# Kernel tuning notes

Measured on AMD Instinct MI355X. Metric: run time of the kernel, lower is better.

Reference implementation:

```python
import jax, jax.numpy as jnp
import numpy as np

N, E, E_LG, H, KGE, NUM_GRAPHS, N_ITER = 100000, 500000, 1000000, 128, 128, 1024, 2
EPS = 1e-5

def _prelu(x, a):
    return jnp.where(x >= 0, x, a * x)

def _seg_mean(vals, idx, num):
    s = jax.ops.segment_sum(vals, idx, num_segments=num)
    c = jax.ops.segment_sum(jnp.ones((vals.shape[0],), vals.dtype), idx, num_segments=num)
    return s / jnp.maximum(c, 1.0)[:, None]

def setup_inputs() -> dict:
    key = jax.random.key(0)
    ks = jax.random.split(key, 16)
    sc = 1.0 / np.sqrt(H)
    inp = {
        "x": jax.random.normal(ks[0], (N, H), jnp.float32),
        "edge_attr": jax.random.normal(ks[1], (E, H), jnp.float32),
        "edge_index": jax.random.randint(ks[2], (2, E), 0, N),
        "batch": jnp.sort(jax.random.randint(ks[3], (N,), 0, NUM_GRAPHS)),
        "line_graph_edge_index": jax.random.randint(ks[4], (2, E_LG), 0, E),
        # edge_update_net: Linear + PReLU + BatchNorm1d (eval mode)
        "W1": jax.random.normal(ks[5], (H, H), jnp.float32) * sc,
        "b1": jnp.zeros((H,), jnp.float32),
        "a1": jnp.full((1,), 0.25, jnp.float32),
        "bn_gamma": jnp.ones((H,), jnp.float32),
        "bn_beta": jnp.zeros((H,), jnp.float32),
        "bn_mean": jnp.zeros((H,), jnp.float32),
        "bn_var": jnp.ones((H,), jnp.float32),
        # GRU (single layer, single step)
        "w_ih": jax.random.normal(ks[6], (3 * H, H), jnp.float32) * sc,
        "w_hh": jax.random.normal(ks[7], (3 * H, H), jnp.float32) * sc,
        "b_ih": jnp.zeros((3 * H,), jnp.float32),
        "b_hh": jnp.zeros((3 * H,), jnp.float32),
        # DynamicAttention net
        "Wa1": jax.random.normal(ks[8], (H // 2, H), jnp.float32) * sc,
        "ba1": jnp.zeros((H // 2,), jnp.float32),
        "a2": jnp.full((1,), 0.25, jnp.float32),
        "Wa2": jax.random.normal(ks[9], (1, H // 2), jnp.float32) * (1.0 / np.sqrt(H // 2)),
        "ba2": jnp.zeros((1,), jnp.float32),
        # readout
        "Wr": jax.random.normal(ks[10], (KGE, H), jnp.float32) * sc,
        "br": jnp.zeros((KGE,), jnp.float32),
    }
    return inp

def reference(x, edge_attr, W1, b1, a1, bn_gamma, bn_beta, bn_mean, bn_var,
              w_ih, w_hh, b_ih, b_hh, Wa1, ba1, a2, Wa2, ba2, Wr, br,
              edge_index, batch, line_graph_edge_index):
    src, dst = edge_index[0], edge_index[1]
    l_src, l_dst = line_graph_edge_index[0], line_graph_edge_index[1]
    h = x  # GRU hidden state [N, H]
    for _ in range(N_ITER):
        # edge-to-edge message passing (node_to_edge_proj is Identity here)
        fused = edge_attr + (x[src] + x[dst]) * 0.5  # [E, H]
        agg = _seg_mean(fused[l_src], l_dst, E)      # scatter-mean over line graph
        upd = _prelu(agg @ W1.T + b1, a1)
        upd = (upd - bn_mean) * jax.lax.rsqrt(bn_var + EPS) * bn_gamma + bn_beta
        fused = fused + upd
        node_updates = _seg_mean(fused, dst, N)      # [N, H]
        # single GRU step
        gi = node_updates @ w_ih.T + b_ih
        gh = h @ w_hh.T + b_hh
        gi_r, gi_z, gi_n = jnp.split(gi, 3, axis=-1)
        gh_r, gh_z, gh_n = jnp.split(gh, 3, axis=-1)
        r = jax.nn.sigmoid(gi_r + gh_r)
        z = jax.nn.sigmoid(gi_z + gh_z)
        n = jnp.tanh(gi_n + r * gh_n)
        h = (1.0 - z) * n + z * h
        x = h
    # dynamic attention: per-graph scalar gate
    graph_repr = _seg_mean(x, batch, NUM_GRAPHS)     # [G, H]
    attn = jax.nn.sigmoid(_prelu(graph_repr @ Wa1.T + ba1, a2) @ Wa2.T + ba2)  # [G, 1]
    attended = x * attn[batch]
    graph_emb = jax.ops.segment_sum(attended, batch, num_segments=NUM_GRAPHS)
    graph_emb = graph_emb @ Wr.T + br
    return (x, graph_emb)
```

## Files before the change

kernel.cpp:

```cpp
#include <hip/hip_runtime.h>
#include <stdint.h>

#define H 128
#define G_NUM 1024
#define BN_EPS 1e-5f
#define IDXCAP 512

typedef unsigned int uint;
typedef unsigned short ushort;
typedef unsigned char uchar;
typedef __attribute__((ext_vector_type(8))) __bf16 bf16x8;
typedef __attribute__((ext_vector_type(8))) ushort ushort8;
typedef __attribute__((ext_vector_type(4))) float f32x4;
typedef __attribute__((ext_vector_type(2))) float f32x2;

__device__ __forceinline__ float b2f(ushort u){ return __uint_as_float(((uint)u) << 16); }
__device__ __forceinline__ ushort f2b(float f){
    uint u = __float_as_uint(f);
    u += 0x7FFFu + ((u >> 16) & 1u);
    return (ushort)(u >> 16);
}
__device__ __forceinline__ float ldf(const void* p, size_t i, int bf){
    return bf ? b2f(((const ushort*)p)[i]) : ((const float*)p)[i];
}
__device__ __forceinline__ int swz(int r, int byte_in_row){
    return (r * 256 + byte_in_row) ^ ((r & 7) << 4);
}

#define GBODY(SRC, sA, sB) do{ \
    uint4 wA_ = *(const uint4*)((SRC) + (size_t)(sA) * H + ch16 * 8); \
    uint4 wB_ = *(const uint4*)((SRC) + (size_t)(sB) * H + ch16 * 8); \
    uint wa_[4] = {wA_.x, wA_.y, wA_.z, wA_.w}; \
    uint wb_[4] = {wB_.x, wB_.y, wB_.z, wB_.w}; \
    _Pragma("unroll") \
    for (int k2 = 0; k2 < 4; k2++){ \
        f32x2 va_, vb_; \
        va_.x = __uint_as_float(wa_[k2] << 16); va_.y = __uint_as_float(wa_[k2] & 0xFFFF0000u); \
        vb_.x = __uint_as_float(wb_[k2] << 16); vb_.y = __uint_as_float(wb_[k2] & 0xFFFF0000u); \
        accA[k2] += va_; accB[k2] += vb_; \
    } }while(0)

__global__ void k_setup_small(const uint* __restrict__ gamma_bits,
                              const void* b1, const void* a1, const void* gam, const void* bet,
                              const void* mean, const void* var, const void* bih, const void* bhh,
                              float* __restrict__ ep, float* __restrict__ bi, float* __restrict__ bh,
                              int* __restrict__ flag, ushort* __restrict__ fz1, ushort* __restrict__ fz2,
                              size_t zoff, int* __restrict__ lg_off, int E, int ELG,
                              int* __restrict__ nd_off, int N, int Etot){
    __shared__ int bfs;
    int t = threadIdx.x;
    if (t == 0){
        int f = (gamma_bits[0] == 0x3F803F80u) ? 1 : 0;
        *flag = f; bfs = f;
        lg_off[E] = ELG;
        nd_off[N] = Etot;
    }
    __syncthreads();
    int bf = bfs;
    bi[t] = ldf(bih, t, bf);
    bh[t] = ldf(bhh, t, bf);
    if (t < 128){
        ep[t]       = ldf(b1, t, bf);
        ep[128 + t] = rsqrtf(ldf(var, t, bf) + BN_EPS) * ldf(gam, t, bf);
        ep[256 + t] = ldf(mean, t, bf);
        ep[384 + t] = ldf(bet, t, bf);
        fz1[zoff + t] = 0; fz2[zoff + t] = 0;
    }
    if (t == 0) ep[512] = ldf(a1, 0, bf);
}

__global__ __launch_bounds__(256) void k_count_nd(const int* __restrict__ ei, int* __restrict__ cnt, int E){
    int t = blockIdx.x * 256 + threadIdx.x;
    if (t < E) atomicAdd(&cnt[ei[E + t]], 1);
}
__global__ __launch_bounds__(256) void k_fill_nd(const int* __restrict__ ei, const int* __restrict__ off,
                                                 int* __restrict__ cur, int* __restrict__ list, int E){
    int t = blockIdx.x * 256 + threadIdx.x;
    if (t >= E) return;
    int k = ei[E + t];
    int pos = atomicAdd(&cur[k], 1);
    list[off[k] + pos] = t;
}
__global__ __launch_bounds__(256) void k_rank(const int* __restrict__ nd_list, int* __restrict__ rank,
                                              int2* __restrict__ eis, const int* __restrict__ ei, int E){
    int j = blockIdx.x * 256 + threadIdx.x;
    if (j >= E) return;
    int e = nd_list[j];
    rank[e] = j;
    eis[j] = make_int2(ei[e], ei[E + e]);
}
__global__ __launch_bounds__(256) void k_count_lg(const int* __restrict__ lgi, const int* __restrict__ rank,
                                                  int* __restrict__ cnt, int ELG){
    int t = blockIdx.x * 256 + threadIdx.x;
    if (t < ELG) atomicAdd(&cnt[rank[lgi[ELG + t]]], 1);
}
__global__ __launch_bounds__(256) void k_fill_lg(const int* __restrict__ lgi, const int* __restrict__ rank,
                                                 const int* __restrict__ off, int* __restrict__ cur,
                                                 int* __restrict__ list, int ELG){
    int t = blockIdx.x * 256 + threadIdx.x;
    if (t >= ELG) return;
    int k = rank[lgi[ELG + t]];
    int pos = atomicAdd(&cur[k], 1);
    list[off[k] + pos] = rank[lgi[t]];
}
__global__ __launch_bounds__(256) void k_scan_reduce(const int* __restrict__ cnt, int* __restrict__ bsum, int n){
    int base = blockIdx.x * 1024;
    int s = 0;
    for (int i = threadIdx.x; i < 1024; i += 256){ int idx = base + i; s += (idx < n) ? cnt[idx] : 0; }
    __shared__ int r[256];
    r[threadIdx.x] = s; __syncthreads();
    for (int o = 128; o > 0; o >>= 1){ if (threadIdx.x < o) r[threadIdx.x] += r[threadIdx.x + o]; __syncthreads(); }
    if (threadIdx.x == 0) bsum[blockIdx.x] = r[0];
}
__global__ __launch_bounds__(256) void k_scan_mid(int* __restrict__ bsum, int nb){
    __shared__ int ts[256];
    int tid = threadIdx.x;
    int loc[4]; int s = 0;
    #pragma unroll
    for (int j = 0; j < 4; j++){
        int idx = tid * 4 + j;
        loc[j] = s;
        s += (idx < nb) ? bsum[idx] : 0;
    }
    ts[tid] = s; __syncthreads();
    for (int o = 1; o < 256; o <<= 1){
        int v = (tid >= o) ? ts[tid - o] : 0;
        __syncthreads();
        ts[tid] += v;
        __syncthreads();
    }
    int texcl = ts[tid] - s;
    #pragma unroll
    for (int j = 0; j < 4; j++){
        int idx = tid * 4 + j;
        if (idx < nb) bsum[idx] = texcl + loc[j];
    }
}
__global__ __launch_bounds__(256) void k_scan_final(const int* __restrict__ cnt, const int* __restrict__ bsum,
                                                    int* __restrict__ off, int n){
    __shared__ int ts[256];
    int base = blockIdx.x * 1024;
    int tid = threadIdx.x;
    int loc[4]; int s = 0;
    #pragma unroll
    for (int j = 0; j < 4; j++){
        int idx = base + tid * 4 + j;
        loc[j] = s;
        s += (idx < n) ? cnt[idx] : 0;
    }
    ts[tid] = s; __syncthreads();
    for (int o = 1; o < 256; o <<= 1){
        int v = (tid >= o) ? ts[tid - o] : 0;
        __syncthreads();
        ts[tid] += v;
        __syncthreads();
    }
    int texcl = ts[tid] - s + bsum[blockIdx.x];
    #pragma unroll
    for (int j = 0; j < 4; j++){
        int idx = base + tid * 4 + j;
        if (idx < n) off[idx] = texcl + loc[j];
    }
}
__global__ __launch_bounds__(256) void k_sortperm(const int* __restrict__ off, uchar* __restrict__ perm, int NK){
    int t = blockIdx.x * 256 + threadIdx.x;
    int wave = t >> 6;
    int l = t & 63;
    int l5 = l & 31;
    int r0 = wave * 32;
    if (r0 >= NK) return;
    int r = r0 + l5;
    int deg = off[r + 1] - off[r];
    int key = (deg << 5) | l5;
    #pragma unroll
    for (int k = 2; k <= 32; k <<= 1){
        #pragma unroll
        for (int j = k >> 1; j > 0; j >>= 1){
            int other = __shfl_xor(key, j);
            bool dir = ((l5 & k) == 0);
            bool lower = ((l5 & j) == 0);
            int mn = min(key, other), mx = max(key, other);
            key = (dir == lower) ? mn : mx;
        }
    }
    if (l < 32) perm[r0 + l5] = (uchar)(key & 31);
}
__global__ __launch_bounds__(256) void k_eaperm(const void* __restrict__ ea, const int* __restrict__ nd_list,
                                                ushort* __restrict__ ea_s, int E, const int* __restrict__ flag){
    int t = blockIdx.x * 256 + threadIdx.x;
    if (t >= E * 16) return;
    int bf = *flag;
    int j = t >> 4, ch = (t & 15) * 8;
    int e = nd_list[j];
    size_t src = (size_t)e * H + ch;
    ushort8 o;
    if (bf){
        o = *(const ushort8*)((const ushort*)ea + src);
    } else {
        float4 a0 = *(const float4*)((const float*)ea + src);
        float4 a1 = *(const float4*)((const float*)ea + src + 4);
        o[0] = f2b(a0.x); o[1] = f2b(a0.y); o[2] = f2b(a0.z); o[3] = f2b(a0.w);
        o[4] = f2b(a1.x); o[5] = f2b(a1.y); o[6] = f2b(a1.z); o[7] = f2b(a1.w);
    }
    *(ushort8*)(ea_s + (size_t)j * H + ch) = o;
}
__global__ __launch_bounds__(256) void k_cvt_bf(const void* __restrict__ in, ushort* __restrict__ out,
                                                int n, const int* __restrict__ flag){
    int t = blockIdx.x * 256 + threadIdx.x;
    if (t >= n) return;
    if (*flag) out[t] = ((const ushort*)in)[t];
    else       out[t] = f2b(((const float*)in)[t]);
}
__global__ __launch_bounds__(256) void k_wcvt(const void* __restrict__ W1, const void* __restrict__ wih,
                                              const void* __restrict__ whh, const void* __restrict__ Wr,
                                              ushort* __restrict__ W1bf, ushort* __restrict__ wihbf,
                                              ushort* __restrict__ whhbf, float* __restrict__ WrT,
                                              const int* __restrict__ flag){
    int t = blockIdx.x * 256 + threadIdx.x;
    int bf = *flag;
    if (t < 16384) W1bf[t] = bf ? ((const ushort*)W1)[t] : f2b(((const float*)W1)[t]);
    else if (t < 65536){ int i = t - 16384; wihbf[i] = bf ? ((const ushort*)wih)[i] : f2b(((const float*)wih)[i]); }
    else if (t < 114688){ int i = t - 65536; whhbf[i] = bf ? ((const ushort*)whh)[i] : f2b(((const float*)whh)[i]); }
    else if (t < 131072){ int i = t - 114688; int r = i >> 7, c = i & 127; WrT[c * 128 + r] = ldf(Wr, i, bf); }
}

__global__ __launch_bounds__(256) void k_fused(const ushort* __restrict__ ea_s, const ushort* __restrict__ hb,
                                               const int2* __restrict__ eis, ushort* __restrict__ fused, int E){
    int t = blockIdx.x * 256 + threadIdx.x;
    if (t >= E * 16) return;
    int j = t >> 4, ch = (t & 15) * 8;
    int2 sd = eis[j];
    size_t base = (size_t)j * H + ch;
    ushort8 hs = *(const ushort8*)(hb + (size_t)sd.x * H + ch);
    ushort8 hd = *(const ushort8*)(hb + (size_t)sd.y * H + ch);
    ushort8 a = *(const ushort8*)(ea_s + base);
    ushort8 o;
    #pragma unroll
    for (int k = 0; k < 8; k++) o[k] = f2b(b2f(a[k]) + 0.5f * (b2f(hs[k]) + b2f(hd[k])));
    *(ushort8*)(fused + base) = o;
}

__global__ __launch_bounds__(256) void k_agg_gemm(const ushort* __restrict__ fused,
                                                  const int* __restrict__ lg_off, const int* __restrict__ list,
                                                  const uchar* __restrict__ perm,
                                                  const ushort* __restrict__ W1bf, const float* __restrict__ ep,
                                                  ushort* __restrict__ fused2, int E, int LMAX){
    __shared__ __attribute__((aligned(16))) char As[32 * 256];
    __shared__ int idxL[IDXCAP];
    __shared__ int offL[33];
    int tid = threadIdx.x, wid = tid >> 6, lane = tid & 63;
    int r0 = blockIdx.x * 32;
    if (tid < 33) offL[tid] = lg_off[r0 + tid];
    __syncthreads();
    int seg_s = offL[0], seglen = offL[32] - seg_s;
    bool staged = (seglen <= IDXCAP);
    if (staged){ for (int j = tid; j < seglen; j += 256) idxL[j] = list[seg_s + j]; }
    __syncthreads();
    int l16 = lane >> 4, ch16 = lane & 15;
    int rA = wid * 8 + l16, rB = rA + 4;
    int plA = perm[r0 + rA], plB = perm[r0 + rB];
    int baseA = offL[plA], degA = offL[plA + 1] - baseA;
    int baseB = offL[plB], degB = offL[plB + 1] - baseB;
    int dm = max(degA, degB);
    #pragma unroll
    for (int o = 32; o > 0; o >>= 1) dm = max(dm, __shfl_xor(dm, o));
    f32x2 accA[4] = {}, accB[4] = {};
    if (staged){
        int relA = baseA - seg_s, relB = baseB - seg_s;
        #pragma unroll 2
        for (int i = 0; i < dm; i++){
            int liA = min(relA + i, seglen - 1);
            int liB = min(relB + i, seglen - 1);
            int sA = idxL[liA];
            int sB = idxL[liB];
            sA = (i < degA) ? sA : E;
            sB = (i < degB) ? sB : E;
            GBODY(fused, sA, sB);
        }
    } else {
        #pragma unroll 2
        for (int i = 0; i < dm; i++){
            int liA = baseA + i; liA = (liA < LMAX) ? liA : (LMAX - 1);
            int liB = baseB + i; liB = (liB < LMAX) ? liB : (LMAX - 1);
            int sA = list[liA];
            int sB = list[liB];
            sA = (i < degA) ? sA : E;
            sB = (i < degB) ? sB : E;
            GBODY(fused, sA, sB);
        }
    }
    float invA = 1.f / fmaxf((float)degA, 1.f);
    float invB = 1.f / fmaxf((float)degB, 1.f);
    ushort8 oA, oB;
    #pragma unroll
    for (int k2 = 0; k2 < 4; k2++){
        oA[2 * k2] = f2b(accA[k2].x * invA); oA[2 * k2 + 1] = f2b(accA[k2].y * invA);
        oB[2 * k2] = f2b(accB[k2].x * invB); oB[2 * k2 + 1] = f2b(accB[k2].y * invB);
    }
    *(ushort8*)(As + swz(plA, ch16 * 16)) = oA;
    *(ushort8*)(As + swz(plB, ch16 * 16)) = oB;
    __syncthreads();
    int lrow = lane & 15, lhi = lane >> 4;
    f32x4 acc[2][2] = {};
    #pragma unroll
    for (int ks = 0; ks < 4; ks++){
        bf16x8 afr[2];
        #pragma unroll
        for (int rt = 0; rt < 2; rt++)
            afr[rt] = *(const bf16x8*)(As + swz(rt * 16 + lrow, ks * 64 + lhi * 16));
        #pragma unroll
        for (int cc = 0; cc < 2; cc++){
            int c = (2 * wid + cc) * 16 + lrow;
            bf16x8 bfr = *(const bf16x8*)(W1bf + (size_t)c * H + ks * 32 + lhi * 8);
            #pragma unroll
            for (int rt = 0; rt < 2; rt++)
                acc[cc][rt] = __builtin_amdgcn_mfma_f32_16x16x32_bf16(afr[rt], bfr, acc[cc][rt], 0, 0, 0);
        }
    }
    __syncthreads();
    float aa = ep[512];
    #pragma unroll
    for (int cc = 0; cc < 2; cc++){
        int c = (2 * wid + cc) * 16 + lrow;
        float bb = ep[c], sc = ep[128 + c], mb = ep[256 + c], be = ep[384 + c];
        #pragma unroll
        for (int rt = 0; rt < 2; rt++)
            #pragma unroll
            for (int rg = 0; rg < 4; rg++){
                int r = rt * 16 + lhi * 4 + rg;
                float u = acc[cc][rt][rg] + bb;
                u = (u >= 0.f) ? u : aa * u;
                u = (u - mb) * sc + be;
                *(ushort*)(As + swz(r, c * 2)) = f2b(u);
            }
    }
    __syncthreads();
    #pragma unroll
    for (int q = 0; q < 2; q++){
        int r = (q == 0) ? rA : rB;
        size_t gbase = (size_t)(r0 + r) * H + ch16 * 8;
        ushort8 f = *(const ushort8*)(fused + gbase);
        ushort8 u = *(const ushort8*)(As + swz(r, ch16 * 16));
        ushort8 o;
        #pragma unroll
        for (int j = 0; j < 8; j++) o[j] = f2b(b2f(f[j]) + b2f(u[j]));
        *(ushort8*)(fused2 + gbase) = o;
    }
}

__global__ __launch_bounds__(256) void k_gru(const ushort* __restrict__ fused2,
                                             const int* __restrict__ nd_off,
                                             const uchar* __restrict__ perm,
                                             ushort* __restrict__ hb,
                                             const ushort* __restrict__ wihbf, const ushort* __restrict__ whhbf,
                                             const float* __restrict__ bi, const float* __restrict__ bh,
                                             int N, int EZ){
    __shared__ __attribute__((aligned(16))) char NUs[32 * 256];
    __shared__ __attribute__((aligned(16))) char HHs[32 * 256];
    __shared__ int offL[33];
    int tid = threadIdx.x, wid = tid >> 6, lane = tid & 63;
    int r0 = blockIdx.x * 32;
    if (tid < 33) offL[tid] = nd_off[r0 + tid];
    int l16 = lane >> 4, ch16 = lane & 15;
    int rA = wid * 8 + l16, rB = rA + 4;
    *(ushort8*)(HHs + swz(rA, ch16 * 16)) = *(const ushort8*)(hb + (size_t)(r0 + rA) * H + ch16 * 8);
    *(ushort8*)(HHs + swz(rB, ch16 * 16)) = *(const ushort8*)(hb + (size_t)(r0 + rB) * H + ch16 * 8);
    __syncthreads();
    int plA = perm[r0 + rA], plB = perm[r0 + rB];
    int baseA = offL[plA], degA = offL[plA + 1] - baseA;
    int baseB = offL[plB], degB = offL[plB + 1] - baseB;
    int dm = max(degA, degB);
    #pragma unroll
    for (int o = 32; o > 0; o >>= 1) dm = max(dm, __shfl_xor(dm, o));
    f32x2 accA[4] = {}, accB[4] = {};
    #pragma unroll 2
    for (int i = 0; i < dm; i++){
        int sA = (i < degA) ? (baseA + i) : EZ;
        int sB = (i < degB) ? (baseB + i) : EZ;
        GBODY(fused2, sA, sB);
    }
    float invA = 1.f / fmaxf((float)degA, 1.f);
    float invB = 1.f / fmaxf((float)degB, 1.f);
    ushort8 oA, oB;
    #pragma unroll
    for (int k2 = 0; k2 < 4; k2++){
        oA[2 * k2] = f2b(accA[k2].x * invA); oA[2 * k2 + 1] = f2b(accA[k2].y * invA);
        oB[2 * k2] = f2b(accB[k2].x * invB); oB[2 * k2 + 1] = f2b(accB[k2].y * invB);
    }
    *(ushort8*)(NUs + swz(plA, ch16 * 16)) = oA;
    *(ushort8*)(NUs + swz(plB, ch16 * 16)) = oB;
    __syncthreads();
    int lrow = lane & 15, lhi = lane >> 4;
    ushort hnew[2][2][4];
    #pragma unroll 1
    for (int b = 0; b < 2; b++){
        f32x4 aI[3][2] = {}, aH[3][2] = {};
        #pragma unroll
        for (int ks = 0; ks < 4; ks++){
            bf16x8 fN[2], fH[2];
            #pragma unroll
            for (int rt = 0; rt < 2; rt++){
                int addr = swz(rt * 16 + lrow, ks * 64 + lhi * 16);
                fN[rt] = *(const bf16x8*)(NUs + addr);
                fH[rt] = *(const bf16x8*)(HHs + addr);
            }
            #pragma unroll
            for (int g = 0; g < 3; g++){
                int c = g * 128 + (wid + 4 * b) * 16 + lrow;
                bf16x8 bI = *(const bf16x8*)(wihbf + (size_t)c * H + ks * 32 + lhi * 8);
                bf16x8 bH = *(const bf16x8*)(whhbf + (size_t)c * H + ks * 32 + lhi * 8);
                #pragma unroll
                for (int rt = 0; rt < 2; rt++){
                    aI[g][rt] = __builtin_amdgcn_mfma_f32_16x16x32_bf16(fN[rt], bI, aI[g][rt], 0, 0, 0);
                    aH[g][rt] = __builtin_amdgcn_mfma_f32_16x16x32_bf16(fH[rt], bH, aH[g][rt], 0, 0, 0);
                }
            }
        }
        int c = (wid + 4 * b) * 16 + lrow;
        float bir = bi[c], biz = bi[128 + c], bin = bi[256 + c];
        float bhr = bh[c], bhz = bh[128 + c], bhn = bh[256 + c];
        #pragma unroll
        for (int rt = 0; rt < 2; rt++)
            #pragma unroll
            for (int rg = 0; rg < 4; rg++){
                int r = rt * 16 + lhi * 4 + rg;
                float gr = aI[0][rt][rg] + bir + aH[0][rt][rg] + bhr;
                float gz = aI[1][rt][rg] + biz + aH[1][rt][rg] + bhz;
                float rv = 1.f / (1.f + __expf(-gr));
                float zv = 1.f / (1.f + __expf(-gz));
                float nv = tanhf(aI[2][rt][rg] + bin + rv * (aH[2][rt][rg] + bhn));
                float hold = b2f(*(const ushort*)(HHs + swz(r, c * 2)));
                hnew[b][rt][rg] = f2b((1.f - zv) * nv + zv * hold);
            }
    }
    __syncthreads();
    #pragma unroll
    for (int b = 0; b < 2; b++){
        int c = (wid + 4 * b) * 16 + lrow;
        #pragma unroll
        for (int rt = 0; rt < 2; rt++)
            #pragma unroll
            for (int rg = 0; rg < 4; rg++){
                int r = rt * 16 + lhi * 4 + rg;
                *(ushort*)(NUs + swz(r, c * 2)) = hnew[b][rt][rg];
            }
    }
    __syncthreads();
    *(ushort8*)(hb + (size_t)(r0 + rA) * H + ch16 * 8) = *(const ushort8*)(NUs + swz(rA, ch16 * 16));
    *(ushort8*)(hb + (size_t)(r0 + rB) * H + ch16 * 8) = *(const ushort8*)(NUs + swz(rB, ch16 * 16));
}

__global__ __launch_bounds__(256) void k_gbounds(const int* __restrict__ batch, int* __restrict__ gs, int N, int G){
    int g = blockIdx.x * 256 + threadIdx.x;
    if (g > G) return;
    int lo = 0, hi = N;
    while (lo < hi){ int mid = (lo + hi) >> 1; if (batch[mid] < g) lo = mid + 1; else hi = mid; }
    gs[g] = lo;
}
__global__ __launch_bounds__(256) void k_graph_sum(const ushort* __restrict__ hb, const int* __restrict__ gs,
                                                   float* __restrict__ gsum, void* __restrict__ out,
                                                   const int* __restrict__ flag){
    int g = blockIdx.x, c = threadIdx.x & 127, half = threadIdx.x >> 7;
    int bf = *flag;
    int s = gs[g], e = gs[g + 1];
    float acc0 = 0.f, acc1 = 0.f;
    int r = s + half;
    for (; r + 2 < e; r += 4){
        ushort u0 = hb[(size_t)r * H + c];
        ushort u1 = hb[(size_t)(r + 2) * H + c];
        float v0 = b2f(u0), v1 = b2f(u1);
        acc0 += v0; acc1 += v1;
        if (bf){ ((ushort*)out)[(size_t)r * H + c] = u0; ((ushort*)out)[(size_t)(r + 2) * H + c] = u1; }
        else   { ((float*) out)[(size_t)r * H + c] = v0; ((float*) out)[(size_t)(r + 2) * H + c] = v1; }
    }
    for (; r < e; r += 2){
        ushort u0 = hb[(size_t)r * H + c];
        float v0 = b2f(u0);
        acc0 += v0;
        if (bf) ((ushort*)out)[(size_t)r * H + c] = u0;
        else    ((float*) out)[(size_t)r * H + c] = v0;
    }
    __shared__ float tmp[128];
    if (half == 1) tmp[c] = acc0 + acc1;
    __syncthreads();
    if (half == 0) gsum[(size_t)g * H + c] = acc0 + acc1 + tmp[c];
}
__global__ void k_attn(const float* __restrict__ gsum, const int* __restrict__ gs,
                       const void* __restrict__ Wa1, const void* __restrict__ ba1,
                       const void* __restrict__ a2, const void* __restrict__ Wa2,
                       const void* __restrict__ ba2, float* __restrict__ attn, const int* __restrict__ flag){
    int g = blockIdx.x;
    int j = threadIdx.x;
    int bf = *flag;
    float inv = 1.0f / fmaxf((float)(gs[g + 1] - gs[g]), 1.0f);
    __shared__ float R[H];
    for (int i = j; i < H; i += 64) R[i] = gsum[(size_t)g * H + i] * inv;
    __syncthreads();
    float t = 0.f;
    for (int k = 0; k < H; k++) t += R[k] * ldf(Wa1, (size_t)j * H + k, bf);
    t += ldf(ba1, j, bf);
    float al = ldf(a2, 0, bf);
    t = (t >= 0.f) ? t : al * t;
    float p = t * ldf(Wa2, j, bf);
    #pragma unroll
    for (int o = 32; o > 0; o >>= 1) p += __shfl_down(p, o);
    if (j == 0) attn[g] = 1.f / (1.f + __expf(-(p + ldf(ba2, 0, bf))));
}
__global__ __launch_bounds__(256) void k_graph_gemm(const float* __restrict__ gsum, const float* __restrict__ attn,
                                                    const float* __restrict__ WrT,
                                                    const void* __restrict__ br, void* __restrict__ out,
                                                    size_t obase, const int* __restrict__ flag){
    __shared__ float A[8 * H];
    int bf = *flag;
    int r0 = blockIdx.x * 8;
    for (int i = threadIdx.x; i < 8 * H; i += 256){
        int r = i >> 7;
        A[i] = gsum[(size_t)(r0 + r) * H + (i & 127)] * attn[r0 + r];
    }
    __syncthreads();
    int c = threadIdx.x & 127;
    int rr = (threadIdx.x >> 7) * 4;
    float acc[4] = {0, 0, 0, 0};
    for (int k = 0; k < H; k++){
        float w = WrT[k * H + c];
        #pragma unroll
        for (int j = 0; j < 4; j++) acc[j] += A[(rr + j) * H + k] * w;
    }
    float bb = ldf(br, c, bf);
    for (int j = 0; j < 4; j++){
        size_t idx = obase + (size_t)(r0 + rr + j) * H + c;
        float v = acc[j] + bb;
        if (bf) ((ushort*)out)[idx] = f2b(v);
        else    ((float*) out)[idx] = v;
    }
}

extern "C" void kernel_launch(void* const* d_in, const int* in_sizes, int n_in,
                              void* d_out, int out_size, void* d_ws, size_t ws_size,
                              hipStream_t stream)
{
    const void* x    = d_in[0];
    const void* ea   = d_in[1];
    const int*  ei   = (const int*)d_in[2];
    const int*  batch= (const int*)d_in[3];
    const int*  lgi  = (const int*)d_in[4];
    const void* W1   = d_in[5];
    const void* b1   = d_in[6];
    const void* a1   = d_in[7];
    const void* bng  = d_in[8];
    const void* bnb  = d_in[9];
    const void* bnm  = d_in[10];
    const void* bnv  = d_in[11];
    const void* wih  = d_in[12];
    const void* whh  = d_in[13];
    const void* bih  = d_in[14];
    const void* bhh  = d_in[15];
    const void* Wa1  = d_in[16];
    const void* ba1  = d_in[17];
    const void* a2   = d_in[18];
    const void* Wa2  = d_in[19];
    const void* ba2  = d_in[20];
    const void* Wr   = d_in[21];
    const void* br   = d_in[22];

    const int N   = in_sizes[0] / H;
    const int E   = in_sizes[1] / H;
    const int ELG = in_sizes[4] / 2;
    const int G   = G_NUM;
    const int nb_lg = (E + 1023) / 1024;
    const int nb_nd = (N + 1023) / 1024;

    char* ws = (char*)d_ws;
    size_t off = 0;
    auto alloc = [&](size_t b) -> void* { void* p = ws + off; off += (b + 255) & ~(size_t)255; return p; };
    int*    flag    = (int*)   alloc(256);
    ushort* hb      = (ushort*)alloc((size_t)N * H * 2);
    ushort* ea_s    = (ushort*)alloc((size_t)E * H * 2);
    ushort* fused   = (ushort*)alloc((size_t)(E + 1) * H * 2);
    ushort* fused2  = (ushort*)alloc((size_t)(E + 1) * H * 2);
    int*    zreg    = (int*)   alloc((size_t)(2 * E + 2 * N) * 4);
    int*    lg_cnt  = zreg;
    int*    lg_cur  = zreg + E;
    int*    nd_cnt  = zreg + 2 * E;
    int*    nd_cur  = zreg + 2 * E + N;
    int*    lg_off  = (int*)   alloc((size_t)(E + 1) * 4);
    int*    nd_off  = (int*)   alloc((size_t)(N + 1) * 4);
    int*    lg_list = (int*)   alloc((size_t)ELG * 4);
    int*    nd_list = (int*)   alloc((size_t)E * 4);
    int*    rank    = (int*)   alloc((size_t)E * 4);
    int2*   eis     = (int2*)  alloc((size_t)E * 8);
    uchar*  perm_lg = (uchar*) alloc((size_t)(E + 32));
    uchar*  perm_nd = (uchar*) alloc((size_t)(N + 32));
    int*    bsumA   = (int*)   alloc((size_t)(nb_lg + 8) * 4);
    int*    bsumB   = (int*)   alloc((size_t)(nb_nd + 8) * 4);
    int*    gs      = (int*)   alloc((size_t)(G + 1) * 4);
    ushort* W1bf    = (ushort*)alloc(128 * 128 * 2);
    ushort* wihbf   = (ushort*)alloc(384 * 128 * 2);
    ushort* whhbf   = (ushort*)alloc(384 * 128 * 2);
    float*  ep      = (float*) alloc(513 * 4);
    float*  bi      = (float*) alloc(384 * 4);
    float*  bh      = (float*) alloc(384 * 4);
    float*  WrT     = (float*) alloc(128 * 128 * 4);
    float*  gsum    = (float*) alloc((size_t)G * H * 4);
    float*  attn    = (float*) alloc((size_t)G * 4);

    k_setup_small<<<1, 384, 0, stream>>>((const uint*)bng, b1, a1, bng, bnb, bnm, bnv, bih, bhh,
                                         ep, bi, bh, flag, fused, fused2, (size_t)E * H,
                                         lg_off, E, ELG, nd_off, N, E);

    hipMemsetAsync(zreg, 0, (size_t)(2 * E + 2 * N) * 4, stream);
    k_count_nd<<<(E + 255) / 256, 256, 0, stream>>>(ei, nd_cnt, E);
    k_scan_reduce<<<nb_nd, 256, 0, stream>>>(nd_cnt, bsumB, N);
    k_scan_mid<<<1, 256, 0, stream>>>(bsumB, nb_nd);
    k_scan_final<<<nb_nd, 256, 0, stream>>>(nd_cnt, bsumB, nd_off, N);
    k_fill_nd<<<(E + 255) / 256, 256, 0, stream>>>(ei, nd_off, nd_cur, nd_list, E);
    k_rank<<<(E + 255) / 256, 256, 0, stream>>>(nd_list, rank, eis, ei, E);
    k_count_lg<<<(ELG + 255) / 256, 256, 0, stream>>>(lgi, rank, lg_cnt, ELG);
    k_scan_reduce<<<nb_lg, 256, 0, stream>>>(lg_cnt, bsumA, E);
    k_scan_mid<<<1, 256, 0, stream>>>(bsumA, nb_lg);
    k_scan_final<<<nb_lg, 256, 0, stream>>>(lg_cnt, bsumA, lg_off, E);
    k_fill_lg<<<(ELG + 255) / 256, 256, 0, stream>>>(lgi, rank, lg_off, lg_cur, lg_list, ELG);
    k_sortperm<<<(E / 32 * 64 + 255) / 256, 256, 0, stream>>>(lg_off, perm_lg, E);
    k_sortperm<<<(N / 32 * 64 + 255) / 256, 256, 0, stream>>>(nd_off, perm_nd, N);
    k_eaperm<<<(E * 16 + 255) / 256, 256, 0, stream>>>(ea, nd_list, ea_s, E, flag);

    k_wcvt<<<(131072 + 255) / 256, 256, 0, stream>>>(W1, wih, whh, Wr, W1bf, wihbf, whhbf, WrT, flag);

    k_cvt_bf<<<(N * H + 255) / 256, 256, 0, stream>>>(x, hb, N * H, flag);

    for (int it = 0; it < 2; it++){
        k_fused<<<(E * 16 + 255) / 256, 256, 0, stream>>>(ea_s, hb, eis, fused, E);
        k_agg_gemm<<<(E + 31) / 32, 256, 0, stream>>>(fused, lg_off, lg_list, perm_lg, W1bf, ep, fused2, E, ELG);
        k_gru<<<(N + 31) / 32, 256, 0, stream>>>(fused2, nd_off, perm_nd, hb, wihbf, whhbf, bi, bh, N, E);
    }

    k_gbounds<<<(G + 256) / 256, 256, 0, stream>>>(batch, gs, N, G);
    k_graph_sum<<<G, 256, 0, stream>>>(hb, gs, gsum, d_out, flag);
    k_attn<<<G, 64, 0, stream>>>(gsum, gs, Wa1, ba1, a2, Wa2, ba2, attn, flag);
    k_graph_gemm<<<G / 8, 256, 0, stream>>>(gsum, attn, WrT, br, d_out, (size_t)N * H, flag);
}
```

Baseline: 1.012 ms.

## Gather edge attributes in fused kernel; split node aggregation from dense GRU

Drops the k_eaperm pre-pass that permuted and converted edge_attr to bf16. k_fused now gathers the original fp32/bf16 edge_attr directly through a new e_orig index, removing one full E×H write and read. The GRU kernel is split into a node-aggregation kernel that writes node updates to global memory and a dense GRU kernel that reloads them. In the dense kernel the r and z input and hidden products share accumulators, and the biases are pre-summed. The trade-off is gathered fp32 edge reads on every iteration, plus an extra N×H round trip and one more launch per iteration.

Result: faster. 964.5 us (-4.7%).

```diff
diff --git a/kernel.cpp b/kernel.cpp
--- a/kernel.cpp
+++ b/kernel.cpp
@@ -82,12 +82,14 @@
     list[off[k] + pos] = t;
 }
 __global__ __launch_bounds__(256) void k_rank(const int* __restrict__ nd_list, int* __restrict__ rank,
-                                              int2* __restrict__ eis, const int* __restrict__ ei, int E){
+                                              int2* __restrict__ eis, int* __restrict__ e_orig,
+                                              const int* __restrict__ ei, int E){
     int j = blockIdx.x * 256 + threadIdx.x;
     if (j >= E) return;
     int e = nd_list[j];
     rank[e] = j;
     eis[j] = make_int2(ei[e], ei[E + e]);
+    e_orig[j] = e;
 }
 __global__ __launch_bounds__(256) void k_count_lg(const int* __restrict__ lgi, const int* __restrict__ rank,
                                                   int* __restrict__ cnt, int ELG){
@@ -185,25 +187,6 @@
     }
     if (l < 32) perm[r0 + l5] = (uchar)(key & 31);
 }
-__global__ __launch_bounds__(256) void k_eaperm(const void* __restrict__ ea, const int* __restrict__ nd_list,
-                                                ushort* __restrict__ ea_s, int E, const int* __restrict__ flag){
-    int t = blockIdx.x * 256 + threadIdx.x;
-    if (t >= E * 16) return;
-    int bf = *flag;
-    int j = t >> 4, ch = (t & 15) * 8;
-    int e = nd_list[j];
-    size_t src = (size_t)e * H + ch;
-    ushort8 o;
-    if (bf){
-        o = *(const ushort8*)((const ushort*)ea + src);
-    } else {
-        float4 a0 = *(const float4*)((const float*)ea + src);
-        float4 a1 = *(const float4*)((const float*)ea + src + 4);
-        o[0] = f2b(a0.x); o[1] = f2b(a0.y); o[2] = f2b(a0.z); o[3] = f2b(a0.w);
-        o[4] = f2b(a1.x); o[5] = f2b(a1.y); o[6] = f2b(a1.z); o[7] = f2b(a1.w);
-    }
-    *(ushort8*)(ea_s + (size_t)j * H + ch) = o;
-}
 __global__ __launch_bounds__(256) void k_cvt_bf(const void* __restrict__ in, ushort* __restrict__ out,
                                                 int n, const int* __restrict__ flag){
     int t = blockIdx.x * 256 + threadIdx.x;
@@ -224,20 +207,33 @@
     else if (t < 131072){ int i = t - 114688; int r = i >> 7, c = i & 127; WrT[c * 128 + r] = ldf(Wr, i, bf); }
 }
 
-__global__ __launch_bounds__(256) void k_fused(const ushort* __restrict__ ea_s, const ushort* __restrict__ hb,
-                                               const int2* __restrict__ eis, ushort* __restrict__ fused, int E){
+__global__ __launch_bounds__(256) void k_fused(const void* __restrict__ ea, const ushort* __restrict__ hb,
+                                               const int2* __restrict__ eis, const int* __restrict__ e_orig,
+                                               ushort* __restrict__ fused, int E, const int* __restrict__ flag){
     int t = blockIdx.x * 256 + threadIdx.x;
     if (t >= E * 16) return;
+    int bf = *flag;
     int j = t >> 4, ch = (t & 15) * 8;
     int2 sd = eis[j];
-    size_t base = (size_t)j * H + ch;
+    int e = e_orig[j];
+    size_t src = (size_t)e * H + ch;
     ushort8 hs = *(const ushort8*)(hb + (size_t)sd.x * H + ch);
     ushort8 hd = *(const ushort8*)(hb + (size_t)sd.y * H + ch);
-    ushort8 a = *(const ushort8*)(ea_s + base);
+    float av[8];
+    if (bf){
+        ushort8 a = *(const ushort8*)((const ushort*)ea + src);
+        #pragma unroll
+        for (int k = 0; k < 8; k++) av[k] = b2f(a[k]);
+    } else {
+        float4 a0 = *(const float4*)((const float*)ea + src);
+        float4 a1 = *(const float4*)((const float*)ea + src + 4);
+        av[0] = a0.x; av[1] = a0.y; av[2] = a0.z; av[3] = a0.w;
+        av[4] = a1.x; av[5] = a1.y; av[6] = a1.z; av[7] = a1.w;
+    }
     ushort8 o;
     #pragma unroll
-    for (int k = 0; k < 8; k++) o[k] = f2b(b2f(a[k]) + 0.5f * (b2f(hs[k]) + b2f(hd[k])));
-    *(ushort8*)(fused + base) = o;
+    for (int k = 0; k < 8; k++) o[k] = f2b(av[k] + 0.5f * (b2f(hs[k]) + b2f(hd[k])));
+    *(ushort8*)(fused + (size_t)j * H + ch) = o;
 }
 
 __global__ __launch_bounds__(256) void k_agg_gemm(const ushort* __restrict__ fused,
@@ -348,24 +344,16 @@
     }
 }
 
-__global__ __launch_bounds__(256) void k_gru(const ushort* __restrict__ fused2,
-                                             const int* __restrict__ nd_off,
-                                             const uchar* __restrict__ perm,
-                                             ushort* __restrict__ hb,
-                                             const ushort* __restrict__ wihbf, const ushort* __restrict__ whhbf,
-                                             const float* __restrict__ bi, const float* __restrict__ bh,
-                                             int N, int EZ){
-    __shared__ __attribute__((aligned(16))) char NUs[32 * 256];
-    __shared__ __attribute__((aligned(16))) char HHs[32 * 256];
+__global__ __launch_bounds__(256) void k_nodeagg(const ushort* __restrict__ fused2,
+                                                 const int* __restrict__ nd_off, const uchar* __restrict__ perm,
+                                                 ushort* __restrict__ NU, int N, int EZ){
     __shared__ int offL[33];
     int tid = threadIdx.x, wid = tid >> 6, lane = tid & 63;
     int r0 = blockIdx.x * 32;
     if (tid < 33) offL[tid] = nd_off[r0 + tid];
+    __syncthreads();
     int l16 = lane >> 4, ch16 = lane & 15;
     int rA = wid * 8 + l16, rB = rA + 4;
-    *(ushort8*)(HHs + swz(rA, ch16 * 16)) = *(const ushort8*)(hb + (size_t)(r0 + rA) * H + ch16 * 8);
-    *(ushort8*)(HHs + swz(rB, ch16 * 16)) = *(const ushort8*)(hb + (size_t)(r0 + rB) * H + ch16 * 8);
-    __syncthreads();
     int plA = perm[r0 + rA], plB = perm[r0 + rB];
     int baseA = offL[plA], degA = offL[plA + 1] - baseA;
     int baseB = offL[plB], degB = offL[plB + 1] - baseB;
@@ -387,14 +375,30 @@
         oA[2 * k2] = f2b(accA[k2].x * invA); oA[2 * k2 + 1] = f2b(accA[k2].y * invA);
         oB[2 * k2] = f2b(accB[k2].x * invB); oB[2 * k2 + 1] = f2b(accB[k2].y * invB);
     }
-    *(ushort8*)(NUs + swz(plA, ch16 * 16)) = oA;
-    *(ushort8*)(NUs + swz(plB, ch16 * 16)) = oB;
+    *(ushort8*)(NU + (size_t)(r0 + plA) * H + ch16 * 8) = oA;
+    *(ushort8*)(NU + (size_t)(r0 + plB) * H + ch16 * 8) = oB;
+}
+
+__global__ __launch_bounds__(256) void k_gru_dense(const ushort* __restrict__ NU_g,
+                                                   ushort* __restrict__ hb,
+                                                   const ushort* __restrict__ wihbf, const ushort* __restrict__ whhbf,
+                                                   const float* __restrict__ bi, const float* __restrict__ bh, int N){
+    __shared__ __attribute__((aligned(16))) char NUs[32 * 256];
+    __shared__ __attribute__((aligned(16))) char HHs[32 * 256];
+    int tid = threadIdx.x, wid = tid >> 6, lane = tid & 63;
+    int r0 = blockIdx.x * 32;
+    int l16 = lane >> 4, ch16 = lane & 15;
+    int rA = wid * 8 + l16, rB = rA + 4;
+    *(ushort8*)(NUs + swz(rA, ch16 * 16)) = *(const ushort8*)(NU_g + (size_t)(r0 + rA) * H + ch16 * 8);
+    *(ushort8*)(NUs + swz(rB, ch16 * 16)) = *(const ushort8*)(NU_g + (size_t)(r0 + rB) * H + ch16 * 8);
+    *(ushort8*)(HHs + swz(rA, ch16 * 16)) = *(const ushort8*)(hb + (size_t)(r0 + rA) * H + ch16 * 8);
+    *(ushort8*)(HHs + swz(rB, ch16 * 16)) = *(const ushort8*)(hb + (size_t)(r0 + rB) * H + ch16 * 8);
     __syncthreads();
     int lrow = lane & 15, lhi = lane >> 4;
     ushort hnew[2][2][4];
     #pragma unroll 1
     for (int b = 0; b < 2; b++){
-        f32x4 aI[3][2] = {}, aH[3][2] = {};
+        f32x4 aR[2] = {}, aZ[2] = {}, aIn[2] = {}, aHn[2] = {};
         #pragma unroll
         for (int ks = 0; ks < 4; ks++){
             bf16x8 fN[2], fH[2];
@@ -404,31 +408,36 @@
                 fN[rt] = *(const bf16x8*)(NUs + addr);
                 fH[rt] = *(const bf16x8*)(HHs + addr);
             }
+            int cb = (wid + 4 * b) * 16 + lrow;
+            size_t wofs = ks * 32 + lhi * 8;
+            bf16x8 wIr = *(const bf16x8*)(wihbf + (size_t)(cb) * H + wofs);
+            bf16x8 wHr = *(const bf16x8*)(whhbf + (size_t)(cb) * H + wofs);
+            bf16x8 wIz = *(const bf16x8*)(wihbf + (size_t)(128 + cb) * H + wofs);
+            bf16x8 wHz = *(const bf16x8*)(whhbf + (size_t)(128 + cb) * H + wofs);
+            bf16x8 wIn_ = *(const bf16x8*)(wihbf + (size_t)(256 + cb) * H + wofs);
+            bf16x8 wHn_ = *(const bf16x8*)(whhbf + (size_t)(256 + cb) * H + wofs);
             #pragma unroll
-            for (int g = 0; g < 3; g++){
-                int c = g * 128 + (wid + 4 * b) * 16 + lrow;
-                bf16x8 bI = *(const bf16x8*)(wihbf + (size_t)c * H + ks * 32 + lhi * 8);
-                bf16x8 bH = *(const bf16x8*)(whhbf + (size_t)c * H + ks * 32 + lhi * 8);
-                #pragma unroll
-                for (int rt = 0; rt < 2; rt++){
-                    aI[g][rt] = __builtin_amdgcn_mfma_f32_16x16x32_bf16(fN[rt], bI, aI[g][rt], 0, 0, 0);
-                    aH[g][rt] = __builtin_amdgcn_mfma_f32_16x16x32_bf16(fH[rt], bH, aH[g][rt], 0, 0, 0);
-                }
+            for (int rt = 0; rt < 2; rt++){
+                aR[rt]  = __builtin_amdgcn_mfma_f32_16x16x32_bf16(fN[rt], wIr,  aR[rt], 0, 0, 0);
+                aR[rt]  = __builtin_amdgcn_mfma_f32_16x16x32_bf16(fH[rt], wHr,  aR[rt], 0, 0, 0);
+                aZ[rt]  = __builtin_amdgcn_mfma_f32_16x16x32_bf16(fN[rt], wIz,  aZ[rt], 0, 0, 0);
+                aZ[rt]  = __builtin_amdgcn_mfma_f32_16x16x32_bf16(fH[rt], wHz,  aZ[rt], 0, 0, 0);
+                aIn[rt] = __builtin_amdgcn_mfma_f32_16x16x32_bf16(fN[rt], wIn_, aIn[rt], 0, 0, 0);
+                aHn[rt] = __builtin_amdgcn_mfma_f32_16x16x32_bf16(fH[rt], wHn_, aHn[rt], 0, 0, 0);
             }
         }
         int c = (wid + 4 * b) * 16 + lrow;
-        float bir = bi[c], biz = bi[128 + c], bin = bi[256 + c];
-        float bhr = bh[c], bhz = bh[128 + c], bhn = bh[256 + c];
+        float brz = bi[c] + bh[c];
+        float bzz = bi[128 + c] + bh[128 + c];
+        float bin = bi[256 + c], bhn = bh[256 + c];
         #pragma unroll
         for (int rt = 0; rt < 2; rt++)
             #pragma unroll
             for (int rg = 0; rg < 4; rg++){
                 int r = rt * 16 + lhi * 4 + rg;
-                float gr = aI[0][rt][rg] + bir + aH[0][rt][rg] + bhr;
-                float gz = aI[1][rt][rg] + biz + aH[1][rt][rg] + bhz;
-                float rv = 1.f / (1.f + __expf(-gr));
-                float zv = 1.f / (1.f + __expf(-gz));
-                float nv = tanhf(aI[2][rt][rg] + bin + rv * (aH[2][rt][rg] + bhn));
+                float rv = 1.f / (1.f + __expf(-(aR[rt][rg] + brz)));
+                float zv = 1.f / (1.f + __expf(-(aZ[rt][rg] + bzz)));
+                float nv = tanhf(aIn[rt][rg] + bin + rv * (aHn[rt][rg] + bhn));
                 float hold = b2f(*(const ushort*)(HHs + swz(r, c * 2)));
                 hnew[b][rt][rg] = f2b((1.f - zv) * nv + zv * hold);
             }
@@ -575,7 +584,7 @@
     auto alloc = [&](size_t b) -> void* { void* p = ws + off; off += (b + 255) & ~(size_t)255; return p; };
     int*    flag    = (int*)   alloc(256);
     ushort* hb      = (ushort*)alloc((size_t)N * H * 2);
-    ushort* ea_s    = (ushort*)alloc((size_t)E * H * 2);
+    ushort* NUb     = (ushort*)alloc((size_t)N * H * 2);
     ushort* fused   = (ushort*)alloc((size_t)(E + 1) * H * 2);
     ushort* fused2  = (ushort*)alloc((size_t)(E + 1) * H * 2);
     int*    zreg    = (int*)   alloc((size_t)(2 * E + 2 * N) * 4);
@@ -589,6 +598,7 @@
     int*    nd_list = (int*)   alloc((size_t)E * 4);
     int*    rank    = (int*)   alloc((size_t)E * 4);
     int2*   eis     = (int2*)  alloc((size_t)E * 8);
+    int*    e_orig  = (int*)   alloc((size_t)E * 4);
     uchar*  perm_lg = (uchar*) alloc((size_t)(E + 32));
     uchar*  perm_nd = (uchar*) alloc((size_t)(N + 32));
     int*    bsumA   = (int*)   alloc((size_t)(nb_lg + 8) * 4);
@@ -614,7 +624,7 @@
     k_scan_mid<<<1, 256, 0, stream>>>(bsumB, nb_nd);
     k_scan_final<<<nb_nd, 256, 0, stream>>>(nd_cnt, bsumB, nd_off, N);
     k_fill_nd<<<(E + 255) / 256, 256, 0, stream>>>(ei, nd_off, nd_cur, nd_list, E);
-    k_rank<<<(E + 255) / 256, 256, 0, stream>>>(nd_list, rank, eis, ei, E);
+    k_rank<<<(E + 255) / 256, 256, 0, stream>>>(nd_list, rank, eis, e_orig, ei, E);
     k_count_lg<<<(ELG + 255) / 256, 256, 0, stream>>>(lgi, rank, lg_cnt, ELG);
     k_scan_reduce<<<nb_lg, 256, 0, stream>>>(lg_cnt, bsumA, E);
     k_scan_mid<<<1, 256, 0, stream>>>(bsumA, nb_lg);
@@ -622,16 +632,16 @@
     k_fill_lg<<<(ELG + 255) / 256, 256, 0, stream>>>(lgi, rank, lg_off, lg_cur, lg_list, ELG);
     k_sortperm<<<(E / 32 * 64 + 255) / 256, 256, 0, stream>>>(lg_off, perm_lg, E);
     k_sortperm<<<(N / 32 * 64 + 255) / 256, 256, 0, stream>>>(nd_off, perm_nd, N);
-    k_eaperm<<<(E * 16 + 255) / 256, 256, 0, stream>>>(ea, nd_list, ea_s, E, flag);
 
     k_wcvt<<<(131072 + 255) / 256, 256, 0, stream>>>(W1, wih, whh, Wr, W1bf, wihbf, whhbf, WrT, flag);
 
     k_cvt_bf<<<(N * H + 255) / 256, 256, 0, stream>>>(x, hb, N * H, flag);
 
     for (int it = 0; it < 2; it++){
-        k_fused<<<(E * 16 + 255) / 256, 256, 0, stream>>>(ea_s, hb, eis, fused, E);
+        k_fused<<<(E * 16 + 255) / 256, 256, 0, stream>>>(ea, hb, eis, e_orig, fused, E, flag);
         k_agg_gemm<<<(E + 31) / 32, 256, 0, stream>>>(fused, lg_off, lg_list, perm_lg, W1bf, ep, fused2, E, ELG);
-        k_gru<<<(N + 31) / 32, 256, 0, stream>>>(fused2, nd_off, perm_nd, hb, wihbf, whhbf, bi, bh, N, E);
+        k_nodeagg<<<(N + 31) / 32, 256, 0, stream>>>(fused2, nd_off, perm_nd, NUb, N, E);
+        k_gru_dense<<<(N + 31) / 32, 256, 0, stream>>>(NUb, hb, wihbf, whhbf, bi, bh, N);
     }
 
     k_gbounds<<<(G + 256) / 256, 256, 0, stream>>>(batch, gs, N, G);
```
